# Kernel tuning notes

Measured on AMD Instinct MI355X. Metric: run time of the kernel, lower is better.

## Reference

```python
import jax, jax.numpy as jnp
import numpy as np

N, E, G = 20000, 320000, 1000
F_NODE, F_EDGE, HID, HEADS, NCLS = 12, 4, 64, 4, 4


def setup_inputs() -> dict:
    key = jax.random.key(0)
    ks = iter(jax.random.split(key, 64))

    def rn(shape, s=0.1):
        return jax.random.normal(next(ks), shape, jnp.float32) * s

    inp = {
        "x": rn((N, F_NODE), 1.0),
        "edge_index": jax.random.randint(next(ks), (2, E), 0, N, dtype=jnp.int32),
        "edge_attr": rn((E, F_EDGE), 1.0),
        "batch": jnp.sort(jax.random.randint(next(ks), (N,), 0, G, dtype=jnp.int32)),
    }
    # GATv2 layer params: lin_l (W,b), lin_r (W,b), lin_edge (W, no bias), att, out bias
    for i, (cin, H) in enumerate([(F_NODE, HEADS), (HID * HEADS, HEADS), (HID * HEADS, 1)], 1):
        d = H * HID
        inp[f"Wl{i}"] = rn((cin, d))
        inp[f"bl{i}"] = rn((d,))
        inp[f"Wr{i}"] = rn((cin, d))
        inp[f"br{i}"] = rn((d,))
        inp[f"We{i}"] = rn((F_EDGE, d))
        inp[f"att{i}"] = rn((H, HID))
        inp[f"bias{i}"] = rn((d,))
    inp["mW1"] = rn((HID, 32)); inp["mb1"] = rn((32,))
    inp["mW2"] = rn((32, 16)); inp["mb2"] = rn((16,))
    inp["mW3"] = rn((16, NCLS)); inp["mb3"] = rn((NCLS,))
    return inp


def gatv2(x, src, dst, ea, Wl, bl, Wr, br, We, att, bias, H):
    # PyG GATv2Conv (share_weights=False, negative_slope=0.2, concat=True, eval mode)
    xl = (x @ Wl + bl).reshape(N, H, HID)   # source transform
    xr = (x @ Wr + br).reshape(N, H, HID)   # target transform
    ee = (ea @ We).reshape(E, H, HID)       # edge embedding
    z = jax.nn.leaky_relu(xl[src] + xr[dst] + ee, 0.2)  # [E,H,C]
    logits = jnp.einsum("ehc,hc->eh", z, att)
    m = jax.ops.segment_max(logits, dst, num_segments=N)  # per-dest max
    ex = jnp.exp(logits - m[dst])
    denom = jax.ops.segment_sum(ex, dst, num_segments=N)
    alpha = ex / (denom[dst] + 1e-16)                      # segment softmax
    msg = (xl[src] * alpha[:, :, None]).reshape(E, H * HID)
    out = jax.ops.segment_sum(msg, dst, num_segments=N)
    return out + bias


def reference(x, edge_index, edge_attr, batch,
              Wl1, bl1, Wr1, br1, We1, att1, bias1,
              Wl2, bl2, Wr2, br2, We2, att2, bias2,
              Wl3, bl3, Wr3, br3, We3, att3, bias3,
              mW1, mb1, mW2, mb2, mW3, mb3):
    src, dst = edge_index[0], edge_index[1]
    h = jax.nn.elu(gatv2(x, src, dst, edge_attr, Wl1, bl1, Wr1, br1, We1, att1, bias1, HEADS))
    h = jax.nn.elu(gatv2(h, src, dst, edge_attr, Wl2, bl2, Wr2, br2, We2, att2, bias2, HEADS))
    h = gatv2(h, src, dst, edge_attr, Wl3, bl3, Wr3, br3, We3, att3, bias3, 1)  # [N,HID]
    # global mean pool
    sums = jax.ops.segment_sum(h, batch, num_segments=G)
    cnt = jax.ops.segment_sum(jnp.ones((N, 1), h.dtype), batch, num_segments=G)
    g = sums / jnp.maximum(cnt, 1.0)
    # MLP head (dropout disabled, eval mode)
    g = jax.nn.relu(g @ mW1 + mb1)
    g = jax.nn.relu(g @ mW2 + mb2)
    return g @ mW3 + mb3
```

## Files before the change

kernel.cpp:

```cpp
#include <hip/hip_runtime.h>
#include <hip/hip_bf16.h>

#define NNODES 20000
#define NEDGES 320000
#define NGRAPH 1000

typedef __hip_bfloat16 bf16;
typedef unsigned short u16;
typedef short short8 __attribute__((ext_vector_type(8)));
typedef float f32x4 __attribute__((ext_vector_type(4)));

__device__ __forceinline__ float b2f(bf16 x) { return __bfloat162float(x); }
__device__ __forceinline__ float bu2f(u16 u) { return __uint_as_float(((unsigned)u) << 16); }
__device__ __forceinline__ u16 f2bu(float v) {
    __hip_bfloat16 b = __float2bfloat16(v);
    return *reinterpret_cast<u16*>(&b);
}

__device__ __forceinline__ int rfl(int v) { return __builtin_amdgcn_readfirstlane(v); }

__device__ __forceinline__ float4 nt_load4(const float* p) {
    f32x4 v = __builtin_nontemporal_load((const f32x4*)p);
    return make_float4(v.x, v.y, v.z, v.w);
}
__device__ __forceinline__ void nt_store4(float* p, float a, float b, float c, float d) {
    f32x4 v = {a, b, c, d};
    __builtin_nontemporal_store(v, (f32x4*)p);
}

__device__ __forceinline__ float rowsum16(float v) {
    v += __int_as_float(__builtin_amdgcn_update_dpp(0, __float_as_int(v), 0x128, 0xF, 0xF, true));
    v += __int_as_float(__builtin_amdgcn_update_dpp(0, __float_as_int(v), 0x124, 0xF, 0xF, true));
    v += __int_as_float(__builtin_amdgcn_update_dpp(0, __float_as_int(v), 0x122, 0xF, 0xF, true));
    v += __int_as_float(__builtin_amdgcn_update_dpp(0, __float_as_int(v), 0x121, 0xF, 0xF, true));
    return v;
}

__device__ __forceinline__ int idx_at(const void* p, int i, int is64) {
    return is64 ? (int)((const long long*)p)[i] : ((const int*)p)[i];
}

__device__ __forceinline__ float raw_at(const void* p, size_t i, bool isbf) {
    return isbf ? b2f(((const bf16*)p)[i]) : ((const float*)p)[i];
}

static inline char* align16(char* p) {
    return (char*)(((uintptr_t)p + 15) & ~(uintptr_t)15);
}

__global__ void sniff_all(const void* __restrict__ x, const void* __restrict__ ei,
                          const void* __restrict__ batch, int* __restrict__ flags) {
    __shared__ int sb[4];
    if (threadIdx.x < 4) sb[threadIdx.x] = 0;
    __syncthreads();
    int gb = 0, gf = 0, ze = 0, zb = 0;
    for (int i = threadIdx.x; i < 8192; i += blockDim.x) {
        float vb = b2f(((const bf16*)x)[i]);
        float vf = ((const float*)x)[i];
        if (fabsf(vb) < 1e4f) gb++;
        if (fabsf(vf) < 1e4f) gf++;
        if (((const int*)ei)[2 * i + 1] == 0) ze++;
        if (((const int*)batch)[2 * i + 1] == 0) zb++;
    }
    atomicAdd(&sb[0], gb); atomicAdd(&sb[1], gf);
    atomicAdd(&sb[2], ze); atomicAdd(&sb[3], zb);
    __syncthreads();
    if (threadIdx.x == 0) {
        flags[0] = (sb[0] >= sb[1]) ? 1 : 0;
        flags[1] = (sb[2] > 6000) ? 1 : 0;
        flags[2] = (sb[3] > 6000) ? 1 : 0;
    }
}

struct Segs {
    const void* src[29];
    int off[30];
};

__device__ __forceinline__ void wtp_store(u16* __restrict__ dst, const void* __restrict__ src,
                                          int K, int N, int i, bool isbf) {
    int j = i & 7;
    int lane = (i >> 3) & 63;
    int rest = i >> 9;
    int KB = K >> 5;
    int tile = rest / KB, kbi = rest - tile * KB;
    int l16 = lane & 15, quad = lane >> 4;
    int n = tile * 16 + l16;
    int kk = kbi * 32 + quad * 8 + j;
    dst[i] = f2bu(raw_at(src, (size_t)kk * N + n, isbf));
}

__global__ void preprocess(Segs S, const int* __restrict__ flags,
                           float* __restrict__ conv, int total,
                           u16* __restrict__ eah,
                           u16* __restrict__ wt2l, u16* __restrict__ wt2r,
                           u16* __restrict__ wt3l, u16* __restrict__ wt3r,
                           int* __restrict__ deg, float* __restrict__ poolcnt) {
    int i = blockIdx.x * blockDim.x + threadIdx.x;
    bool isbf = flags[0] != 0;
    if (i < total) {
        int lo = 0, hi = 29;
        while (hi - lo > 1) {
            int mid = (lo + hi) >> 1;
            if (i >= S.off[mid]) lo = mid; else hi = mid;
        }
        conv[i] = raw_at(S.src[lo], i - S.off[lo], isbf);
        return;
    }
    i -= total;
    if (i < NEDGES * 4) {
        eah[i] = isbf ? ((const u16*)S.src[1])[i] : f2bu(((const float*)S.src[1])[i]);
        return;
    }
    i -= NEDGES * 4;
    if (i < 65536) { wtp_store(wt2l, S.src[9],  256, 256, i, isbf); return; }
    i -= 65536;
    if (i < 65536) { wtp_store(wt2r, S.src[11], 256, 256, i, isbf); return; }
    i -= 65536;
    if (i < 16384) { wtp_store(wt3l, S.src[16], 256, 64, i, isbf); return; }
    i -= 16384;
    if (i < 16384) { wtp_store(wt3r, S.src[18], 256, 64, i, isbf); return; }
    i -= 16384;
    if (i < NNODES) { deg[i] = 0; return; }
    i -= NNODES;
    if (i < NGRAPH * 65) poolcnt[i] = 0.f;
}

__global__ void csr_hist(const void* __restrict__ ei, const int* __restrict__ flags,
                         int* __restrict__ deg) {
    int e = blockIdx.x * blockDim.x + threadIdx.x;
    if (e >= NEDGES) return;
    atomicAdd(&deg[idx_at(ei, NEDGES + e, flags[1])], 1);
}

__global__ void csr_scan(const int* __restrict__ deg, int* __restrict__ rowptr,
                         int* __restrict__ cursor) {
    __shared__ int wsum[16];
    __shared__ int wpre[16];
    const int t = threadIdx.x;
    const int wid = t >> 6, lane = t & 63;
    const int base = t * 20;
    int loc[20];
    int s = 0;
#pragma unroll
    for (int j = 0; j < 20; j++) {
        int i = base + j;
        int v = (i < NNODES) ? deg[i] : 0;
        loc[j] = s;
        s += v;
    }
    int incl = s;
#pragma unroll
    for (int o = 1; o < 64; o <<= 1) {
        int n = __shfl_up(incl, o);
        if (lane >= o) incl += n;
    }
    if (lane == 63) wsum[wid] = incl;
    __syncthreads();
    if (wid == 0 && lane < 16) {
        int v = wsum[lane];
        int inc2 = v;
#pragma unroll
        for (int o = 1; o < 16; o <<= 1) {
            int n = __shfl_up(inc2, o);
            if (lane >= o) inc2 += n;
        }
        wpre[lane] = inc2 - v;
    }
    __syncthreads();
    int excl = wpre[wid] + incl - s;
#pragma unroll
    for (int j = 0; j < 20; j++) {
        int i = base + j;
        if (i < NNODES) { rowptr[i] = excl + loc[j]; cursor[i] = excl + loc[j]; }
    }
    if (t == 1023) rowptr[NNODES] = excl + s;
}

__global__ void csr_scatter(const void* __restrict__ ei, const int* __restrict__ flags,
                            int* __restrict__ cursor, int2* __restrict__ csr) {
    int e = blockIdx.x * blockDim.x + threadIdx.x;
    if (e >= NEDGES) return;
    const int i64 = flags[1];
    int src = idx_at(ei, e, i64), dst = idx_at(ei, NEDGES + e, i64);
    int pos = atomicAdd(&cursor[dst], 1);
    csr[pos] = make_int2(src, e);
}

template <int TM, int CIN, int DOUT, bool GUARD>
__global__ __launch_bounds__(256, 2) void lin_gemm(
        const float* __restrict__ X,
        const float* __restrict__ Wl, const float* __restrict__ bl,
        const float* __restrict__ Wr, const float* __restrict__ br,
        u16* __restrict__ XL, float* __restrict__ XR) {
    constexpr int CPT = DOUT / 4;
    constexpr int RG = 256 / CPT;
    constexpr int M = RG * TM;
    __shared__ float xs[M * CIN];

    const int t = threadIdx.x;
    const int ct = t % CPT;
    const int rg = t / CPT;
    const int c0 = ct * 4;
    const int r0 = blockIdx.x * M;

    constexpr int C4 = CIN / 4;
    for (int i = t; i < M * C4; i += 256) {
        int r = i / C4, j = i - r * C4;
        float4 v = make_float4(0.f, 0.f, 0.f, 0.f);
        if (!GUARD || (r0 + r) < NNODES)
            v = *(const float4*)&X[(size_t)(r0 + r) * CIN + j * 4];
        *(float4*)&xs[r * CIN + j * 4] = v;
    }
    __syncthreads();

    float4 accL[TM], accR[TM];
#pragma unroll
    for (int m = 0; m < TM; m++) {
        accL[m] = make_float4(0.f, 0.f, 0.f, 0.f);
        accR[m] = make_float4(0.f, 0.f, 0.f, 0.f);
    }
    const float* xbase = &xs[rg * TM * CIN];
#pragma unroll 4
    for (int k = 0; k < CIN; k++) {
        const float4 wl = *(const float4*)&Wl[k * DOUT + c0];
        const float4 wr = *(const float4*)&Wr[k * DOUT + c0];
#pragma unroll
        for (int m = 0; m < TM; m++) {
            float xv = xbase[m * CIN + k];
            accL[m].x = fmaf(xv, wl.x, accL[m].x);
            accL[m].y = fmaf(xv, wl.y, accL[m].y);
            accL[m].z = fmaf(xv, wl.z, accL[m].z);
            accL[m].w = fmaf(xv, wl.w, accL[m].w);
            accR[m].x = fmaf(xv, wr.x, accR[m].x);
            accR[m].y = fmaf(xv, wr.y, accR[m].y);
            accR[m].z = fmaf(xv, wr.z, accR[m].z);
            accR[m].w = fmaf(xv, wr.w, accR[m].w);
        }
    }

    const float4 b4l = *(const float4*)&bl[c0];
    const float4 b4r = *(const float4*)&br[c0];
#pragma unroll
    for (int m = 0; m < TM; m++) {
        int row = r0 + rg * TM + m;
        if (GUARD && row >= NNODES) continue;
        float l0 = accL[m].x + b4l.x, l1 = accL[m].y + b4l.y;
        float l2 = accL[m].z + b4l.z, l3 = accL[m].w + b4l.w;
        uint2 pk;
        pk.x = (unsigned)f2bu(l0) | ((unsigned)f2bu(l1) << 16);
        pk.y = (unsigned)f2bu(l2) | ((unsigned)f2bu(l3) << 16);
        *(uint2*)&XL[(size_t)row * DOUT + c0] = pk;
        nt_store4(&XR[(size_t)row * DOUT + c0],
                  accR[m].x + b4r.x, accR[m].y + b4r.y,
                  accR[m].z + b4r.z, accR[m].w + b4r.w);
    }
}

template <int N>
__global__ __launch_bounds__(256) void lin_gemm_mfma(
        const float* __restrict__ X,
        const u16* __restrict__ WlP, const float* __restrict__ bl,
        const u16* __restrict__ WrP, const float* __restrict__ br,
        u16* __restrict__ XL, float* __restrict__ XR) {
    constexpr int K = 256;
    constexpr int KB = K / 32;
    constexpr int NTW = N / 64;
    constexpr int XSTR = 264;
    __shared__ u16 xhi[16 * XSTR];
    __shared__ u16 xlo[16 * XSTR];

    const int t = threadIdx.x;
    const int w = t >> 6, lane = t & 63;
    const int quad = lane >> 4, l16 = lane & 15;
    const int m0 = blockIdx.x * 16;
    const int nbase = w * (N / 4);

    for (int idx = t; idx < 16 * 64; idx += 256) {
        int r = idx >> 6, c4 = idx & 63;
        float4 v = *(const float4*)&X[(size_t)(m0 + r) * K + c4 * 4];
        float f[4] = {v.x, v.y, v.z, v.w};
        ushort4 hi, lo;
        u16 h;
        h = f2bu(f[0]); hi.x = h; lo.x = f2bu(f[0] - bu2f(h));
        h = f2bu(f[1]); hi.y = h; lo.y = f2bu(f[1] - bu2f(h));
        h = f2bu(f[2]); hi.z = h; lo.z = f2bu(f[2] - bu2f(h));
        h = f2bu(f[3]); hi.w = h; lo.w = f2bu(f[3] - bu2f(h));
        *(ushort4*)&xhi[r * XSTR + c4 * 4] = hi;
        *(ushort4*)&xlo[r * XSTR + c4 * 4] = lo;
    }
    __syncthreads();

    f32x4 accL[NTW], accR[NTW];
#pragma unroll
    for (int i = 0; i < NTW; i++) {
        accL[i] = (f32x4){0.f, 0.f, 0.f, 0.f};
        accR[i] = (f32x4){0.f, 0.f, 0.f, 0.f};
    }

    const int abase = l16 * XSTR + quad * 8;
#pragma unroll
    for (int kbi = 0; kbi < KB; kbi++) {
        short8 ahi = *(const short8*)&xhi[abase + kbi * 32];
        short8 alo = *(const short8*)&xlo[abase + kbi * 32];
#pragma unroll
        for (int i = 0; i < NTW; i++) {
            int tg = (nbase >> 4) + i;
            size_t off = ((size_t)(tg * KB + kbi) * 64 + lane) * 8;
            short8 bL = *(const short8*)&WlP[off];
            short8 bR = *(const short8*)&WrP[off];
            accL[i] = __builtin_amdgcn_mfma_f32_16x16x32_bf16(ahi, bL, accL[i], 0, 0, 0);
            accL[i] = __builtin_amdgcn_mfma_f32_16x16x32_bf16(alo, bL, accL[i], 0, 0, 0);
            accR[i] = __builtin_amdgcn_mfma_f32_16x16x32_bf16(ahi, bR, accR[i], 0, 0, 0);
            accR[i] = __builtin_amdgcn_mfma_f32_16x16x32_bf16(alo, bR, accR[i], 0, 0, 0);
        }
    }

#pragma unroll
    for (int i = 0; i < NTW; i++) {
        int col = nbase + i * 16 + l16;
        float bLv = bl[col], bRv = br[col];
#pragma unroll
        for (int r = 0; r < 4; r++) {
            int row = m0 + quad * 4 + r;
            XL[(size_t)row * N + col] = f2bu(accL[i][r] + bLv);
            __builtin_nontemporal_store(accR[i][r] + bRv, &XR[(size_t)row * N + col]);
        }
    }
}

template <bool ELU>
__global__ __launch_bounds__(256, 2) void gat_agg_mw(
        const int* __restrict__ rowptr, const int2* __restrict__ csr,
        const u16* __restrict__ XL, const float* __restrict__ XR,
        const u16* __restrict__ eah,
        const float* __restrict__ We, const float* __restrict__ att,
        const float* __restrict__ bias, float* __restrict__ out) {
    const int lane = threadIdx.x & 63;
    const int dst = rfl(blockIdx.x * 4 + (threadIdx.x >> 6));
    const int c0 = lane * 4;

    const float4 w0 = *(const float4*)&We[0 * 256 + c0];
    const float4 w1 = *(const float4*)&We[1 * 256 + c0];
    const float4 w2 = *(const float4*)&We[2 * 256 + c0];
    const float4 w3 = *(const float4*)&We[3 * 256 + c0];
    const float4 at = *(const float4*)&att[c0];
    const float4 xr = nt_load4(&XR[(size_t)dst * 256 + c0]);
    const uint2* __restrict__ eah2 = (const uint2*)eah;

    const int i0 = rfl(rowptr[dst]);
    const int i1 = rfl(rowptr[dst + 1]);

    float l = 0.f;
    float4 acc = make_float4(0.f, 0.f, 0.f, 0.f);

#define MW_BODY(XU, A0, A1, A2, A3)                                              \
    {                                                                            \
        float xl0 = __uint_as_float((XU).x << 16);                               \
        float xl1 = __uint_as_float((XU).x & 0xffff0000u);                       \
        float xl2 = __uint_as_float((XU).y << 16);                               \
        float xl3 = __uint_as_float((XU).y & 0xffff0000u);                       \
        float z0 = fmaf(A0, w0.x, fmaf(A1, w1.x, fmaf(A2, w2.x, fmaf(A3, w3.x, xl0 + xr.x)))); \
        float z1 = fmaf(A0, w0.y, fmaf(A1, w1.y, fmaf(A2, w2.y, fmaf(A3, w3.y, xl1 + xr.y)))); \
        float z2 = fmaf(A0, w0.z, fmaf(A1, w1.z, fmaf(A2, w2.z, fmaf(A3, w3.z, xl2 + xr.z)))); \
        float z3 = fmaf(A0, w0.w, fmaf(A1, w1.w, fmaf(A2, w2.w, fmaf(A3, w3.w, xl3 + xr.w)))); \
        z0 = fmaxf(z0, 0.2f * z0);                                               \
        z1 = fmaxf(z1, 0.2f * z1);                                               \
        z2 = fmaxf(z2, 0.2f * z2);                                               \
        z3 = fmaxf(z3, 0.2f * z3);                                               \
        float v = fmaf(z3, at.w, fmaf(z2, at.z, fmaf(z1, at.y, z0 * at.x)));     \
        v = rowsum16(v);                                                         \
        float p = __expf(v);                                                     \
        l += p;                                                                  \
        acc.x = fmaf(p, xl0, acc.x);                                             \
        acc.y = fmaf(p, xl1, acc.y);                                             \
        acc.z = fmaf(p, xl2, acc.z);                                             \
        acc.w = fmaf(p, xl3, acc.w);                                             \
    }

#define MW_LOAD(K)                                                               \
        int2 t##K = csr[e + K];                                                  \
        int sx##K = rfl(t##K.x), sy##K = rfl(t##K.y);                            \
        uint2 xu##K = *(const uint2*)&XL[(size_t)sx##K * 256 + c0];              \
        uint2 au##K = eah2[sy##K];                                               \
        float a##K##0 = __uint_as_float(rfl(au##K.x << 16));                     \
        float a##K##1 = __uint_as_float(rfl(au##K.x & 0xffff0000u));             \
        float a##K##2 = __uint_as_float(rfl(au##K.y << 16));                     \
        float a##K##3 = __uint_as_float(rfl(au##K.y & 0xffff0000u));

    int e = i0;
    for (; e + 8 <= i1; e += 8) {
        MW_LOAD(0) MW_LOAD(1) MW_LOAD(2) MW_LOAD(3)
        MW_LOAD(4) MW_LOAD(5) MW_LOAD(6) MW_LOAD(7)
        MW_BODY(xu0, a00, a01, a02, a03)
        MW_BODY(xu1, a10, a11, a12, a13)
        MW_BODY(xu2, a20, a21, a22, a23)
        MW_BODY(xu3, a30, a31, a32, a33)
        MW_BODY(xu4, a40, a41, a42, a43)
        MW_BODY(xu5, a50, a51, a52, a53)
        MW_BODY(xu6, a60, a61, a62, a63)
        MW_BODY(xu7, a70, a71, a72, a73)
    }
    for (; e + 4 <= i1; e += 4) {
        MW_LOAD(0) MW_LOAD(1) MW_LOAD(2) MW_LOAD(3)
        MW_BODY(xu0, a00, a01, a02, a03)
        MW_BODY(xu1, a10, a11, a12, a13)
        MW_BODY(xu2, a20, a21, a22, a23)
        MW_BODY(xu3, a30, a31, a32, a33)
    }
    for (; e < i1; ++e) {
        MW_LOAD(0)
        MW_BODY(xu0, a00, a01, a02, a03)
    }
#undef MW_LOAD
#undef MW_BODY

    float inv = 1.f / (l + 1e-16f);
    const float4 b4 = *(const float4*)&bias[c0];
    float o0 = fmaf(acc.x, inv, b4.x);
    float o1 = fmaf(acc.y, inv, b4.y);
    float o2 = fmaf(acc.z, inv, b4.z);
    float o3 = fmaf(acc.w, inv, b4.w);
    if (ELU) {
        o0 = o0 > 0.f ? o0 : expf(o0) - 1.f;
        o1 = o1 > 0.f ? o1 : expf(o1) - 1.f;
        o2 = o2 > 0.f ? o2 : expf(o2) - 1.f;
        o3 = o3 > 0.f ? o3 : expf(o3) - 1.f;
    }
    nt_store4(&out[(size_t)dst * 256 + c0], o0, o1, o2, o3);
}

template <bool ELU>
__global__ __launch_bounds__(256, 4) void gat_agg4(
                        const int* __restrict__ rowptr, const int2* __restrict__ csr,
                        const u16* __restrict__ XL, const float* __restrict__ XR,
                        const u16* __restrict__ eah,
                        const float* __restrict__ We, const float* __restrict__ att,
                        const float* __restrict__ bias, float* __restrict__ out) {
    const int t = threadIdx.x;
    const int lane = t & 63;
    const int g = lane >> 4;
    const int k = lane & 15;
    const int c0 = k * 4;
    const int dst = rfl(blockIdx.x * 4 + (t >> 6));

    const float4 w0 = *(const float4*)&We[0 * 64 + c0];
    const float4 w1 = *(const float4*)&We[1 * 64 + c0];
    const float4 w2 = *(const float4*)&We[2 * 64 + c0];
    const float4 w3 = *(const float4*)&We[3 * 64 + c0];
    const float4 at = *(const float4*)&att[c0];
    const float4 xr = nt_load4(&XR[(size_t)dst * 64 + c0]);
    const uint2* __restrict__ eah2 = (const uint2*)eah;

    const int i0 = rfl(rowptr[dst]);
    const int i1 = rfl(rowptr[dst + 1]);
    const int niter = (i1 - i0 + 3) >> 2;

    float l = 0.f;
    float4 acc = make_float4(0.f, 0.f, 0.f, 0.f);

#define G4_BODY(E_IDX)                                                           \
    {                                                                            \
        int e_ = (E_IDX);                                                        \
        bool valid_ = e_ < i1;                                                   \
        int2 se_ = csr[valid_ ? e_ : i0];                                        \
        uint2 xu_ = *(const uint2*)&XL[(size_t)se_.x * 64 + c0];                 \
        uint2 au_ = eah2[se_.y];                                                 \
        float xl0_ = __uint_as_float(xu_.x << 16);                               \
        float xl1_ = __uint_as_float(xu_.x & 0xffff0000u);                       \
        float xl2_ = __uint_as_float(xu_.y << 16);                               \
        float xl3_ = __uint_as_float(xu_.y & 0xffff0000u);                       \
        float A0_ = __uint_as_float(au_.x << 16);                                \
        float A1_ = __uint_as_float(au_.x & 0xffff0000u);                        \
        float A2_ = __uint_as_float(au_.y << 16);                                \
        float A3_ = __uint_as_float(au_.y & 0xffff0000u);                        \
        float z0_ = fmaf(A0_, w0.x, fmaf(A1_, w1.x, fmaf(A2_, w2.x, fmaf(A3_, w3.x, xl0_ + xr.x)))); \
        float z1_ = fmaf(A0_, w0.y, fmaf(A1_, w1.y, fmaf(A2_, w2.y, fmaf(A3_, w3.y, xl1_ + xr.y)))); \
        float z2_ = fmaf(A0_, w0.z, fmaf(A1_, w1.z, fmaf(A2_, w2.z, fmaf(A3_, w3.z, xl2_ + xr.z)))); \
        float z3_ = fmaf(A0_, w0.w, fmaf(A1_, w1.w, fmaf(A2_, w2.w, fmaf(A3_, w3.w, xl3_ + xr.w)))); \
        z0_ = fmaxf(z0_, 0.2f * z0_);                                            \
        z1_ = fmaxf(z1_, 0.2f * z1_);                                            \
        z2_ = fmaxf(z2_, 0.2f * z2_);                                            \
        z3_ = fmaxf(z3_, 0.2f * z3_);                                            \
        float v_ = fmaf(z3_, at.w, fmaf(z2_, at.z, fmaf(z1_, at.y, z0_ * at.x))); \
        v_ = rowsum16(v_);                                                       \
        float p_ = valid_ ? __expf(v_) : 0.f;                                    \
        l += p_;                                                                 \
        acc.x = fmaf(p_, xl0_, acc.x);                                           \
        acc.y = fmaf(p_, xl1_, acc.y);                                           \
        acc.z = fmaf(p_, xl2_, acc.z);                                           \
        acc.w = fmaf(p_, xl3_, acc.w);                                           \
    }

    int it = 0;
    for (; it + 2 <= niter; it += 2) {
        int eb = i0 + g + it * 4;
        G4_BODY(eb)
        G4_BODY(eb + 4)
    }
    if (it < niter) {
        G4_BODY(i0 + g + it * 4)
    }
#undef G4_BODY

    l += __shfl_xor(l, 16);      l += __shfl_xor(l, 32);
    acc.x += __shfl_xor(acc.x, 16); acc.x += __shfl_xor(acc.x, 32);
    acc.y += __shfl_xor(acc.y, 16); acc.y += __shfl_xor(acc.y, 32);
    acc.z += __shfl_xor(acc.z, 16); acc.z += __shfl_xor(acc.z, 32);
    acc.w += __shfl_xor(acc.w, 16); acc.w += __shfl_xor(acc.w, 32);

    if (g == 0) {
        float inv = 1.f / (l + 1e-16f);
        const float4 b4 = *(const float4*)&bias[c0];
        float o0 = fmaf(acc.x, inv, b4.x);
        float o1 = fmaf(acc.y, inv, b4.y);
        float o2 = fmaf(acc.z, inv, b4.z);
        float o3 = fmaf(acc.w, inv, b4.w);
        if (ELU) {
            o0 = o0 > 0.f ? o0 : expf(o0) - 1.f;
            o1 = o1 > 0.f ? o1 : expf(o1) - 1.f;
            o2 = o2 > 0.f ? o2 : expf(o2) - 1.f;
            o3 = o3 > 0.f ? o3 : expf(o3) - 1.f;
        }
        nt_store4(&out[(size_t)dst * 64 + c0], o0, o1, o2, o3);
    }
}

__global__ void pool_mlp(const float* __restrict__ h,
                         const void* __restrict__ batch, const int* __restrict__ flags,
                         const float* __restrict__ mW1, const float* __restrict__ mb1,
                         const float* __restrict__ mW2, const float* __restrict__ mb2,
                         const float* __restrict__ mW3, const float* __restrict__ mb3,
                         float* __restrict__ out) {
    __shared__ int se[2];
    __shared__ float g[64], s1[32], s2[16];
    const int b = blockIdx.x, t = threadIdx.x;
    const int is64 = flags[2];
    if (t < 2) {
        int target = b + t;
        int lo = 0, hi = NNODES;
        while (lo < hi) {
            int mid = (lo + hi) >> 1;
            if (idx_at(batch, mid, is64) < target) lo = mid + 1; else hi = mid;
        }
        se[t] = lo;
    }
    __syncthreads();
    const int s = se[0], e = se[1];
    float a = 0.f;
    for (int i = s; i < e; i++) a += h[(size_t)i * 64 + t];
    g[t] = a / fmaxf((float)(e - s), 1.f);
    __syncthreads();
    if (t < 32) {
        float acc = 0.f;
        for (int k = 0; k < 64; k++) acc = fmaf(g[k], mW1[k * 32 + t], acc);
        s1[t] = fmaxf(acc + mb1[t], 0.f);
    }
    __syncthreads();
    if (t < 16) {
        float acc = 0.f;
        for (int k = 0; k < 32; k++) acc = fmaf(s1[k], mW2[k * 16 + t], acc);
        s2[t] = fmaxf(acc + mb2[t], 0.f);
    }
    __syncthreads();
    if (t < 4) {
        float acc = 0.f;
        for (int k = 0; k < 16; k++) acc = fmaf(s2[k], mW3[k * 4 + t], acc);
        out[b * 4 + t] = acc + mb3[t];
    }
}


extern "C" void kernel_launch(void* const* d_in, const int* in_sizes, int n_in,
                              void* d_out, int out_size, void* d_ws, size_t ws_size,
                              hipStream_t stream) {
    const void* ei    = d_in[1];
    const void* batch = d_in[3];

    int fidx[29];
    fidx[0] = 0;
    fidx[1] = 2;
    for (int i = 0; i < 21; i++) fidx[2 + i] = 4 + i;
    for (int i = 0; i < 6; i++) fidx[23 + i] = 25 + i;

    Segs S;
    int off = 0;
    for (int i = 0; i < 29; i++) {
        S.src[i] = d_in[fidx[i]];
        S.off[i] = off;
        off += in_sizes[fidx[i]];
    }
    S.off[29] = off;
    const int total = off;

    char* p = (char*)d_ws;
    int*   FLAGS  = (int*)p;                 p += 16;
    float* CONV   = (float*)p;               p += sizeof(float) * total;  p = align16(p);
    int*   DEG    = (int*)p;                 p += sizeof(int) * NNODES;
    int*   ROWPTR = (int*)p;                 p += sizeof(int) * (NNODES + 1);
    int*   CURSOR = (int*)p;                 p += sizeof(int) * (NNODES + 1);  p = align16(p);
    int2*  CSR    = (int2*)p;                p += sizeof(int2) * NEDGES;  p = align16(p);
    u16*   EAH    = (u16*)p;                 p += sizeof(u16) * NEDGES * 4;  p = align16(p);
    u16*   WT2L   = (u16*)p;                 p += sizeof(u16) * 256 * 256;
    u16*   WT2R   = (u16*)p;                 p += sizeof(u16) * 256 * 256;
    u16*   WT3L   = (u16*)p;                 p += sizeof(u16) * 64 * 256;
    u16*   WT3R   = (u16*)p;                 p += sizeof(u16) * 64 * 256;  p = align16(p);
    u16*   XLb    = (u16*)p;                 p += sizeof(u16) * NNODES * 256;  p = align16(p);
    float* XRb    = (float*)p;               p += sizeof(float) * NNODES * 256;
    float* ACC    = (float*)p;               p += sizeof(float) * NNODES * 256;
    float* POOL   = (float*)p;               p += sizeof(float) * NGRAPH * 64;
    float* CNT    = (float*)p;               p += sizeof(float) * NGRAPH;

    const float* CX  = CONV + S.off[0];
    const float* CP[21];
    for (int i = 0; i < 21; i++) CP[i] = CONV + S.off[2 + i];
    const float* CmW1 = CONV + S.off[23];
    const float* Cmb1 = CONV + S.off[24];
    const float* CmW2 = CONV + S.off[25];
    const float* Cmb2 = CONV + S.off[26];
    const float* CmW3 = CONV + S.off[27];
    const float* Cmb3 = CONV + S.off[28];

    sniff_all<<<1, 256, 0, stream>>>(d_in[0], ei, batch, FLAGS);
    int pre_total = total + NEDGES * 4 + 65536 * 2 + 16384 * 2 + NNODES + NGRAPH * 65;
    preprocess<<<(pre_total + 255) / 256, 256, 0, stream>>>(
        S, FLAGS, CONV, total, EAH, WT2L, WT2R, WT3L, WT3R, DEG, POOL);

    csr_hist<<<(NEDGES + 255) / 256, 256, 0, stream>>>(ei, FLAGS, DEG);
    csr_scan<<<1, 1024, 0, stream>>>(DEG, ROWPTR, CURSOR);
    csr_scatter<<<(NEDGES + 255) / 256, 256, 0, stream>>>(ei, FLAGS, CURSOR, CSR);

    lin_gemm<4, 12, 256, false><<<NNODES / 16, 256, 0, stream>>>(CX, CP[0], CP[1], CP[2], CP[3], XLb, XRb);
    gat_agg_mw<true><<<NNODES / 4, 256, 0, stream>>>(ROWPTR, CSR, XLb, XRb, EAH,
        CP[4], CP[5], CP[6], ACC);

    lin_gemm_mfma<256><<<NNODES / 16, 256, 0, stream>>>(ACC, WT2L, CP[8], WT2R, CP[10], XLb, XRb);
    gat_agg_mw<true><<<NNODES / 4, 256, 0, stream>>>(ROWPTR, CSR, XLb, XRb, EAH,
        CP[11], CP[12], CP[13], ACC);

    lin_gemm_mfma<64><<<NNODES / 16, 256, 0, stream>>>(ACC, WT3L, CP[15], WT3R, CP[17], XLb, XRb);
    gat_agg4<false><<<NNODES / 4, 256, 0, stream>>>(ROWPTR, CSR, XLb, XRb, EAH,
        CP[18], CP[19], CP[20], ACC);

    pool_mlp<<<NGRAPH, 64, 0, stream>>>(ACC, batch, FLAGS,
        CmW1, Cmb1, CmW2, Cmb2, CmW3, Cmb3, (float*)d_out);
}
```

Before: 370.0 us.

## Pack bf16 edge attributes into CSR entries and drop nontemporal loads/stores

The CSR entry grows from int2 (src, edge id) to int4 (src, packed bf16 edge attributes), so the aggregation kernels no longer do a second, dependent gather into the edge-attribute array for each edge. The scatter kernel reads the edge attributes once and writes them in dst-sorted order. Separately, every nontemporal load and store of XR and the output is replaced by a plain access, which lets the next kernel find that data in cache. The cost is a CSR array twice as large, with four bytes of padding per entry.

```diff
diff --git a/kernel.cpp b/kernel.cpp
--- a/kernel.cpp
+++ b/kernel.cpp
@@ -18,15 +18,6 @@
 }
 
 __device__ __forceinline__ int rfl(int v) { return __builtin_amdgcn_readfirstlane(v); }
-
-__device__ __forceinline__ float4 nt_load4(const float* p) {
-    f32x4 v = __builtin_nontemporal_load((const f32x4*)p);
-    return make_float4(v.x, v.y, v.z, v.w);
-}
-__device__ __forceinline__ void nt_store4(float* p, float a, float b, float c, float d) {
-    f32x4 v = {a, b, c, d};
-    __builtin_nontemporal_store(v, (f32x4*)p);
-}
 
 __device__ __forceinline__ float rowsum16(float v) {
     v += __int_as_float(__builtin_amdgcn_update_dpp(0, __float_as_int(v), 0x128, 0xF, 0xF, true));
@@ -178,13 +169,15 @@
 }
 
 __global__ void csr_scatter(const void* __restrict__ ei, const int* __restrict__ flags,
-                            int* __restrict__ cursor, int2* __restrict__ csr) {
+                            const u16* __restrict__ eah,
+                            int* __restrict__ cursor, int4* __restrict__ csr) {
     int e = blockIdx.x * blockDim.x + threadIdx.x;
     if (e >= NEDGES) return;
     const int i64 = flags[1];
     int src = idx_at(ei, e, i64), dst = idx_at(ei, NEDGES + e, i64);
+    uint2 au = *(const uint2*)&eah[(size_t)e * 4];
     int pos = atomicAdd(&cursor[dst], 1);
-    csr[pos] = make_int2(src, e);
+    csr[pos] = make_int4(src, (int)au.x, (int)au.y, 0);
 }
 
 template <int TM, int CIN, int DOUT, bool GUARD>
@@ -251,9 +244,10 @@
         pk.x = (unsigned)f2bu(l0) | ((unsigned)f2bu(l1) << 16);
         pk.y = (unsigned)f2bu(l2) | ((unsigned)f2bu(l3) << 16);
         *(uint2*)&XL[(size_t)row * DOUT + c0] = pk;
-        nt_store4(&XR[(size_t)row * DOUT + c0],
-                  accR[m].x + b4r.x, accR[m].y + b4r.y,
-                  accR[m].z + b4r.z, accR[m].w + b4r.w);
+        float4 r4;
+        r4.x = accR[m].x + b4r.x; r4.y = accR[m].y + b4r.y;
+        r4.z = accR[m].z + b4r.z; r4.w = accR[m].w + b4r.w;
+        *(float4*)&XR[(size_t)row * DOUT + c0] = r4;
     }
 }
 
@@ -324,16 +318,15 @@
         for (int r = 0; r < 4; r++) {
             int row = m0 + quad * 4 + r;
             XL[(size_t)row * N + col] = f2bu(accL[i][r] + bLv);
-            __builtin_nontemporal_store(accR[i][r] + bRv, &XR[(size_t)row * N + col]);
+            XR[(size_t)row * N + col] = accR[i][r] + bRv;
         }
     }
 }
 
 template <bool ELU>
 __global__ __launch_bounds__(256, 2) void gat_agg_mw(
-        const int* __restrict__ rowptr, const int2* __restrict__ csr,
+        const int* __restrict__ rowptr, const int4* __restrict__ csr,
         const u16* __restrict__ XL, const float* __restrict__ XR,
-        const u16* __restrict__ eah,
         const float* __restrict__ We, const float* __restrict__ att,
         const float* __restrict__ bias, float* __restrict__ out) {
     const int lane = threadIdx.x & 63;
@@ -345,8 +338,7 @@
     const float4 w2 = *(const float4*)&We[2 * 256 + c0];
     const float4 w3 = *(const float4*)&We[3 * 256 + c0];
     const float4 at = *(const float4*)&att[c0];
-    const float4 xr = nt_load4(&XR[(size_t)dst * 256 + c0]);
-    const uint2* __restrict__ eah2 = (const uint2*)eah;
+    const float4 xr = *(const float4*)&XR[(size_t)dst * 256 + c0];
 
     const int i0 = rfl(rowptr[dst]);
     const int i1 = rfl(rowptr[dst + 1]);
@@ -379,14 +371,13 @@
     }
 
 #define MW_LOAD(K)                                                               \
-        int2 t##K = csr[e + K];                                                  \
-        int sx##K = rfl(t##K.x), sy##K = rfl(t##K.y);                            \
+        int4 t##K = csr[e + K];                                                  \
+        int sx##K = rfl(t##K.x);                                                 \
         uint2 xu##K = *(const uint2*)&XL[(size_t)sx##K * 256 + c0];              \
-        uint2 au##K = eah2[sy##K];                                               \
-        float a##K##0 = __uint_as_float(rfl(au##K.x << 16));                     \
-        float a##K##1 = __uint_as_float(rfl(au##K.x & 0xffff0000u));             \
-        float a##K##2 = __uint_as_float(rfl(au##K.y << 16));                     \
-        float a##K##3 = __uint_as_float(rfl(au##K.y & 0xffff0000u));
+        float a##K##0 = __uint_as_float(rfl((int)((unsigned)t##K.y << 16)));     \
+        float a##K##1 = __uint_as_float(rfl((int)((unsigned)t##K.y & 0xffff0000u))); \
+        float a##K##2 = __uint_as_float(rfl((int)((unsigned)t##K.z << 16)));     \
+        float a##K##3 = __uint_as_float(rfl((int)((unsigned)t##K.z & 0xffff0000u)));
 
     int e = i0;
     for (; e + 8 <= i1; e += 8) {
@@ -427,14 +418,13 @@
         o2 = o2 > 0.f ? o2 : expf(o2) - 1.f;
         o3 = o3 > 0.f ? o3 : expf(o3) - 1.f;
     }
-    nt_store4(&out[(size_t)dst * 256 + c0], o0, o1, o2, o3);
+    *(float4*)&out[(size_t)dst * 256 + c0] = make_float4(o0, o1, o2, o3);
 }
 
 template <bool ELU>
 __global__ __launch_bounds__(256, 4) void gat_agg4(
-                        const int* __restrict__ rowptr, const int2* __restrict__ csr,
+                        const int* __restrict__ rowptr, const int4* __restrict__ csr,
                         const u16* __restrict__ XL, const float* __restrict__ XR,
-                        const u16* __restrict__ eah,
                         const float* __restrict__ We, const float* __restrict__ att,
                         const float* __restrict__ bias, float* __restrict__ out) {
     const int t = threadIdx.x;
@@ -449,8 +439,7 @@
     const float4 w2 = *(const float4*)&We[2 * 64 + c0];
     const float4 w3 = *(const float4*)&We[3 * 64 + c0];
     const float4 at = *(const float4*)&att[c0];
-    const float4 xr = nt_load4(&XR[(size_t)dst * 64 + c0]);
-    const uint2* __restrict__ eah2 = (const uint2*)eah;
+    const float4 xr = *(const float4*)&XR[(size_t)dst * 64 + c0];
 
     const int i0 = rfl(rowptr[dst]);
     const int i1 = rfl(rowptr[dst + 1]);
@@ -463,17 +452,16 @@
     {                                                                            \
         int e_ = (E_IDX);                                                        \
         bool valid_ = e_ < i1;                                                   \
-        int2 se_ = csr[valid_ ? e_ : i0];                                        \
+        int4 se_ = csr[valid_ ? e_ : i0];                                        \
         uint2 xu_ = *(const uint2*)&XL[(size_t)se_.x * 64 + c0];                 \
-        uint2 au_ = eah2[se_.y];                                                 \
         float xl0_ = __uint_as_float(xu_.x << 16);                               \
         float xl1_ = __uint_as_float(xu_.x & 0xffff0000u);                       \
         float xl2_ = __uint_as_float(xu_.y << 16);                               \
         float xl3_ = __uint_as_float(xu_.y & 0xffff0000u);                       \
-        float A0_ = __uint_as_float(au_.x << 16);                                \
-        float A1_ = __uint_as_float(au_.x & 0xffff0000u);                        \
-        float A2_ = __uint_as_float(au_.y << 16);                                \
-        float A3_ = __uint_as_float(au_.y & 0xffff0000u);                        \
+        float A0_ = __uint_as_float((unsigned)se_.y << 16);                      \
+        float A1_ = __uint_as_float((unsigned)se_.y & 0xffff0000u);              \
+        float A2_ = __uint_as_float((unsigned)se_.z << 16);                      \
+        float A3_ = __uint_as_float((unsigned)se_.z & 0xffff0000u);              \
         float z0_ = fmaf(A0_, w0.x, fmaf(A1_, w1.x, fmaf(A2_, w2.x, fmaf(A3_, w3.x, xl0_ + xr.x)))); \
         float z1_ = fmaf(A0_, w0.y, fmaf(A1_, w1.y, fmaf(A2_, w2.y, fmaf(A3_, w3.y, xl1_ + xr.y)))); \
         float z2_ = fmaf(A0_, w0.z, fmaf(A1_, w1.z, fmaf(A2_, w2.z, fmaf(A3_, w3.z, xl2_ + xr.z)))); \
@@ -522,7 +510,7 @@
             o2 = o2 > 0.f ? o2 : expf(o2) - 1.f;
             o3 = o3 > 0.f ? o3 : expf(o3) - 1.f;
         }
-        nt_store4(&out[(size_t)dst * 64 + c0], o0, o1, o2, o3);
+        *(float4*)&out[(size_t)dst * 64 + c0] = make_float4(o0, o1, o2, o3);
     }
 }
 
@@ -599,7 +587,7 @@
     int*   DEG    = (int*)p;                 p += sizeof(int) * NNODES;
     int*   ROWPTR = (int*)p;                 p += sizeof(int) * (NNODES + 1);
     int*   CURSOR = (int*)p;                 p += sizeof(int) * (NNODES + 1);  p = align16(p);
-    int2*  CSR    = (int2*)p;                p += sizeof(int2) * NEDGES;  p = align16(p);
+    int4*  CSR    = (int4*)p;                p += sizeof(int4) * NEDGES;  p = align16(p);
     u16*   EAH    = (u16*)p;                 p += sizeof(u16) * NEDGES * 4;  p = align16(p);
     u16*   WT2L   = (u16*)p;                 p += sizeof(u16) * 256 * 256;
     u16*   WT2R   = (u16*)p;                 p += sizeof(u16) * 256 * 256;
@@ -628,18 +616,18 @@
 
     csr_hist<<<(NEDGES + 255) / 256, 256, 0, stream>>>(ei, FLAGS, DEG);
     csr_scan<<<1, 1024, 0, stream>>>(DEG, ROWPTR, CURSOR);
-    csr_scatter<<<(NEDGES + 255) / 256, 256, 0, stream>>>(ei, FLAGS, CURSOR, CSR);
+    csr_scatter<<<(NEDGES + 255) / 256, 256, 0, stream>>>(ei, FLAGS, EAH, CURSOR, CSR);
 
     lin_gemm<4, 12, 256, false><<<NNODES / 16, 256, 0, stream>>>(CX, CP[0], CP[1], CP[2], CP[3], XLb, XRb);
-    gat_agg_mw<true><<<NNODES / 4, 256, 0, stream>>>(ROWPTR, CSR, XLb, XRb, EAH,
+    gat_agg_mw<true><<<NNODES / 4, 256, 0, stream>>>(ROWPTR, CSR, XLb, XRb,
         CP[4], CP[5], CP[6], ACC);
 
     lin_gemm_mfma<256><<<NNODES / 16, 256, 0, stream>>>(ACC, WT2L, CP[8], WT2R, CP[10], XLb, XRb);
-    gat_agg_mw<true><<<NNODES / 4, 256, 0, stream>>>(ROWPTR, CSR, XLb, XRb, EAH,
+    gat_agg_mw<true><<<NNODES / 4, 256, 0, stream>>>(ROWPTR, CSR, XLb, XRb,
         CP[11], CP[12], CP[13], ACC);
 
     lin_gemm_mfma<64><<<NNODES / 16, 256, 0, stream>>>(ACC, WT3L, CP[15], WT3R, CP[17], XLb, XRb);
-    gat_agg4<false><<<NNODES / 4, 256, 0, stream>>>(ROWPTR, CSR, XLb, XRb, EAH,
+    gat_agg4<false><<<NNODES / 4, 256, 0, stream>>>(ROWPTR, CSR, XLb, XRb,
         CP[18], CP[19], CP[20], ACC);
 
     pool_mlp<<<NGRAPH, 64, 0, stream>>>(ACC, batch, FLAGS,
```

New measurement: 351.1 us. 1.05x faster.
